# Kernel optimization log

Hardware: AMD Instinct MI355X
Metric: run time of the kernel (lower is better)

The kernel has to match this reference:

```python
import jax, jax.numpy as jnp
import numpy as np

N_IN, N_OUT, D_IN, D_HID, STYLE = 16384, 16384, 64, 256, 64
E = 1048576
EPS_BN = 1e-5
EPS_ADA = 1e-8
SLOPE = 0.2

def leaky(x):
    return jnp.where(x >= 0, x, SLOPE * x)

def bn_train(h, g, b):
    # BatchNorm1d, training mode: batch stats over dim 0, biased variance
    m = jnp.mean(h, axis=0)
    v = jnp.var(h, axis=0)
    return (h - m) * jax.lax.rsqrt(v + EPS_BN) * g + b

def adain(h, style, w1, b1, w2, b2):
    # per-node instance norm over feature axis (unbiased std, as torch.std),
    # style-conditioned per-feature gamma/beta
    mean = jnp.mean(h, axis=1, keepdims=True)
    std = jnp.std(h, axis=1, ddof=1, keepdims=True)
    gamma = w1 @ style + b1
    beta = w2 @ style + b2
    return gamma * (h - mean) / (std + EPS_ADA) + beta

def gat_conv(h, src, dst, W, att_src, att_dst, bias):
    # PyG GATConv, heads=1: linear -> edge attention -> segment softmax -> scatter
    xs = h @ W.T                          # [N, D_IN]
    a_s = xs @ att_src                    # [N]
    a_d = xs @ att_dst                    # [N]
    e = leaky(a_s[src] + a_d[dst])        # [E]
    emax = jax.ops.segment_max(e, dst, num_segments=N_OUT)
    emax = jnp.where(jnp.isfinite(emax), emax, 0.0)
    ex = jnp.exp(e - emax[dst])
    den = jax.ops.segment_sum(ex, dst, num_segments=N_OUT)
    alpha = ex / den[dst]                 # softmax over incoming edges per dst
    out = jax.ops.segment_sum(alpha[:, None] * xs[src], dst, num_segments=N_OUT)
    return out + bias

def setup_inputs():
    key = jax.random.key(0)
    ks = jax.random.split(key, 24)
    p = lambda k, shape: jax.random.normal(k, shape, jnp.float32) * 0.05
    return {
        "x": jax.random.normal(ks[0], (N_IN, D_IN), jnp.float32),
        "style": jax.random.normal(ks[1], (STYLE,), jnp.float32),
        "edge_index": jax.random.randint(ks[2], (2, E), 0, N_OUT, jnp.int32),
        "trs_w": p(ks[3], (N_OUT, N_IN)), "trs_b": jnp.zeros((N_OUT,), jnp.float32),
        "bn2_g": jnp.ones((N_OUT,), jnp.float32), "bn2_b": jnp.zeros((N_OUT,), jnp.float32),
        "fc1_w": p(ks[4], (D_HID, D_IN)), "fc1_b": jnp.zeros((D_HID,), jnp.float32),
        "bn1_g": jnp.ones((D_HID,), jnp.float32), "bn1_b": jnp.zeros((D_HID,), jnp.float32),
        "gat_w": p(ks[5], (D_IN, D_HID)),
        "gat_att_src": p(ks[6], (D_IN,)), "gat_att_dst": p(ks[7], (D_IN,)),
        "gat_b": jnp.zeros((D_IN,), jnp.float32),
        "a1_w1": p(ks[8], (D_IN, STYLE)), "a1_b1": jnp.zeros((D_IN,), jnp.float32),
        "a1_w2": p(ks[9], (D_IN, STYLE)), "a1_b2": jnp.zeros((D_IN,), jnp.float32),
        "a2_w1": p(ks[10], (D_HID, STYLE)), "a2_b1": jnp.zeros((D_HID,), jnp.float32),
        "a2_w2": p(ks[11], (D_HID, STYLE)), "a2_b2": jnp.zeros((D_HID,), jnp.float32),
        "a3_w1": p(ks[12], (D_IN, STYLE)), "a3_b1": jnp.zeros((D_IN,), jnp.float32),
        "a3_w2": p(ks[13], (D_IN, STYLE)), "a3_b2": jnp.zeros((D_IN,), jnp.float32),
    }

def reference(x, style, edge_index, trs_w, trs_b, bn2_g, bn2_b, fc1_w, fc1_b, bn1_g, bn1_b, gat_w, gat_att_src, gat_att_dst, gat_b, a1_w1, a1_b1, a1_w2, a1_b2, a2_w1, a2_b1, a2_w2, a2_b2, a3_w1, a3_b1, a3_w2, a3_b2):
    h = x.T @ trs_w.T + trs_b                 # [D_IN, N_OUT]
    h = leaky(bn_train(h, bn2_g, bn2_b))      # dropout: eval-mode identity
    h = h.T                                    # [N_OUT, D_IN]
    h = adain(h, style, a1_w1, a1_b1, a1_w2, a1_b2)
    h = leaky(bn_train(h @ fc1_w.T + fc1_b, bn1_g, bn1_b))  # [N_OUT, D_HID]
    h = adain(h, style, a2_w1, a2_b1, a2_w2, a2_b2)
    src, dst = edge_index[0], edge_index[1]
    h = leaky(gat_conv(h, src, dst, gat_w, gat_att_src, gat_att_dst, gat_b))
    h = adain(h, style, a3_w1, a3_b1, a3_w2, a3_b2)
    return h
```

## Files before the change

### kernel.cpp

```cpp
#include <hip/hip_runtime.h>
#include <hip/hip_bf16.h>

#define N_NODES 16384
#define NEDGE   1048576

typedef __attribute__((ext_vector_type(4))) float f32x4;
typedef __attribute__((ext_vector_type(4))) unsigned u32x4;
typedef __attribute__((ext_vector_type(8))) short bf16x8;
typedef unsigned short u16;

__device__ __forceinline__ short f2bf(float f) {
  union { float f; unsigned u; } v; v.f = f;
  unsigned r = v.u + 0x7FFFu + ((v.u >> 16) & 1u);
  return (short)(r >> 16);
}
__device__ __forceinline__ unsigned pk2(float lo, float hi) {
  __hip_bfloat162 h = __float22bfloat162_rn(make_float2(lo, hi));
  return *reinterpret_cast<unsigned*>(&h);
}
__device__ __forceinline__ bf16x8 cvt8(f32x4 a, f32x4 b) {
  u32x4 u;
  u[0] = pk2(a[0], a[1]); u[1] = pk2(a[2], a[3]);
  u[2] = pk2(b[0], b[1]); u[3] = pk2(b[2], b[3]);
  return __builtin_bit_cast(bf16x8, u);
}
__device__ __forceinline__ float red16(float v) {
  v += __shfl_xor(v, 1); v += __shfl_xor(v, 2);
  v += __shfl_xor(v, 4); v += __shfl_xor(v, 8);
  return v;
}
__device__ __forceinline__ float red64(float v) {
  v += __shfl_xor(v, 1); v += __shfl_xor(v, 2); v += __shfl_xor(v, 4);
  v += __shfl_xor(v, 8); v += __shfl_xor(v, 16); v += __shfl_xor(v, 32);
  return v;
}
__device__ __forceinline__ float lrelu(float x){ return x >= 0.f ? x : 0.2f*x; }

__global__ __launch_bounds__(256) void k_prep(
    const float* __restrict__ x, const float* __restrict__ style,
    const float* __restrict__ fc1_w, const float* __restrict__ gat_w,
    const float* __restrict__ a1w1, const float* __restrict__ a1b1,
    const float* __restrict__ a1w2, const float* __restrict__ a1b2,
    const float* __restrict__ a2w1, const float* __restrict__ a2b1,
    const float* __restrict__ a2w2, const float* __restrict__ a2b2,
    const float* __restrict__ a3w1, const float* __restrict__ a3b1,
    const float* __restrict__ a3w2, const float* __restrict__ a3b2,
    u16* __restrict__ xpk, u16* __restrict__ fc1pk, u16* __restrict__ gatpk,
    float* __restrict__ gb, int* __restrict__ cnt,
    float* __restrict__ colsum, float* __restrict__ colsq)
{
  int tid = blockIdx.x * 256 + threadIdx.x;
  if (tid < 131072) {
    int lane = tid & 63;
    int kt = tid >> 8, nt = (tid >> 6) & 3;
    int k0 = kt*32 + (lane>>4)*8, c = nt*16 + (lane&15);
    bf16x8 o;
    #pragma unroll
    for (int j = 0; j < 8; ++j) o[j] = f2bf(x[(size_t)(k0+j)*64 + c]);
    ((bf16x8*)xpk)[tid] = o;
  } else if (tid < 133120) {
    int t2 = tid - 131072;
    int lane = t2 & 63, kt = t2 >> 10, nt = (t2 >> 6) & 15;
    int k0 = kt*32 + (lane>>4)*8, c = nt*16 + (lane&15);
    bf16x8 o;
    #pragma unroll
    for (int j = 0; j < 8; ++j) o[j] = f2bf(fc1_w[(size_t)c*64 + k0 + j]);
    ((bf16x8*)fc1pk)[t2] = o;
  } else if (tid < 135168) {
    int t3 = tid - 133120;
    int lane = t3 & 63, kt = t3 >> 8, nt = (t3 >> 6) & 3;
    int k0 = kt*32 + (lane>>4)*8, c = nt*16 + (lane&15);
    bf16x8 o;
    #pragma unroll
    for (int j = 0; j < 8; ++j) o[j] = f2bf(gat_w[(size_t)c*256 + k0 + j]);
    ((bf16x8*)gatpk)[t3] = o;
  } else if (tid < 135936) {
    int t4 = tid - 135168;
    const float* wp; const float* bp; float* op; int d;
    if (t4 < 64)       { wp=a1w1; bp=a1b1; op=gb;       d=t4; }
    else if (t4 < 128) { wp=a1w2; bp=a1b2; op=gb+64;    d=t4-64; }
    else if (t4 < 384) { wp=a2w1; bp=a2b1; op=gb+128;   d=t4-128; }
    else if (t4 < 640) { wp=a2w2; bp=a2b2; op=gb+384;   d=t4-384; }
    else if (t4 < 704) { wp=a3w1; bp=a3b1; op=gb+640;   d=t4-640; }
    else               { wp=a3w2; bp=a3b2; op=gb+704;   d=t4-704; }
    float s = bp[d];
    for (int k = 0; k < 64; ++k) s += wp[(size_t)d*64 + k] * style[k];
    op[d] = s;
  } else if (tid < 152320) {
    cnt[tid - 135936] = 0;
  } else if (tid < 152832) {
    int t6 = tid - 152320;
    if (t6 < 256) colsum[t6] = 0.f; else colsq[t6-256] = 0.f;
  }
}

__global__ __launch_bounds__(256, 4) void k_gemm12(
    const float* __restrict__ W, const u16* __restrict__ xpk,
    const float* __restrict__ trs_b, const float* __restrict__ bn2_g,
    const float* __restrict__ bn2_b, const float* __restrict__ g1,
    const float* __restrict__ be1,
    const u16* __restrict__ fc1pk, const float* __restrict__ fc1_b,
    float* __restrict__ H3, float* __restrict__ colsum, float* __restrict__ colsq,
    const int* __restrict__ dst, int* __restrict__ cnt)
{
  if (blockIdx.x >= 1024) {
    int t = ((blockIdx.x - 1024) << 8) + threadIdx.x;
    #pragma unroll
    for (int i = 0; i < 4; ++i) atomicAdd(&cnt[dst[t + i*262144]], 1);
    return;
  }
  const int lane = threadIdx.x & 63;
  const int wv   = threadIdx.x >> 6;
  const int jb   = blockIdx.x << 4;
  const int c0   = lane & 15, kg = lane >> 4;
  const int kt0  = wv << 7;
  const f32x4* __restrict__ apv =
      (const f32x4*)(W + (size_t)(jb + c0) * 16384 + (size_t)kt0 * 32 + kg * 8);
  const bf16x8* __restrict__ bpv = ((const bf16x8*)xpk) + (size_t)kt0 * 256 + lane;
  f32x4 z = {0.f,0.f,0.f,0.f};
  f32x4 acc0 = z, acc1 = z, acc2 = z, acc3 = z;
  #pragma unroll 2
  for (int t = 0; t < 128; ++t) {
    f32x4 a0 = __builtin_nontemporal_load(apv);
    f32x4 a1 = __builtin_nontemporal_load(apv + 1);
    bf16x8 b0 = bpv[0];
    bf16x8 b1 = bpv[64];
    bf16x8 b2 = bpv[128];
    bf16x8 b3 = bpv[192];
    bf16x8 a = cvt8(a0, a1);
    acc0 = __builtin_amdgcn_mfma_f32_16x16x32_bf16(a, b0, acc0, 0, 0, 0);
    acc1 = __builtin_amdgcn_mfma_f32_16x16x32_bf16(a, b1, acc1, 0, 0, 0);
    acc2 = __builtin_amdgcn_mfma_f32_16x16x32_bf16(a, b2, acc2, 0, 0, 0);
    acc3 = __builtin_amdgcn_mfma_f32_16x16x32_bf16(a, b3, acc3, 0, 0, 0);
    apv += 8; bpv += 256;
  }
  __shared__ float lred[4 * 16 * 64];
  __shared__ float h2t[16 * 68];
  {
    float* rp = lred + (wv << 10) + lane;
    #pragma unroll
    for (int nt = 0; nt < 4; ++nt) {
      f32x4 a = nt==0?acc0:nt==1?acc1:nt==2?acc2:acc3;
      #pragma unroll
      for (int r = 0; r < 4; ++r) rp[((nt<<2)+r)<<6] = a[r];
    }
  }
  __syncthreads();
  if (wv == 0) {
    float val[4][4];
    const float* rp = lred + lane;
    #pragma unroll
    for (int nt = 0; nt < 4; ++nt)
      #pragma unroll
      for (int r = 0; r < 4; ++r) {
        int idx = ((nt<<2)+r)<<6;
        val[nt][r] = rp[idx] + rp[idx+1024] + rp[idx+2048] + rp[idx+3072];
      }
    #pragma unroll
    for (int r = 0; r < 4; ++r) {
      int jr = (kg << 2) + r;
      int j  = jb + jr;
      float tb = trs_b[j];
      float v0 = val[0][r]+tb, v1 = val[1][r]+tb, v2 = val[2][r]+tb, v3 = val[3][r]+tb;
      float s = red16(v0+v1+v2+v3);
      float q = red16(v0*v0+v1*v1+v2*v2+v3*v3);
      float mean = s * 0.015625f;
      float var  = q * 0.015625f - mean*mean;
      float inv  = rsqrtf(var + 1e-5f) * bn2_g[j];
      float bb   = bn2_b[j];
      v0 = lrelu((v0-mean)*inv + bb); v1 = lrelu((v1-mean)*inv + bb);
      v2 = lrelu((v2-mean)*inv + bb); v3 = lrelu((v3-mean)*inv + bb);
      s = red16(v0+v1+v2+v3);
      q = red16(v0*v0+v1*v1+v2*v2+v3*v3);
      mean = s * 0.015625f;
      var  = q * 0.015625f - mean*mean;
      float sd = sqrtf(fmaxf(var, 0.f) * (64.f/63.f));
      float id = 1.f / (sd + 1e-8f);
      float* hr = h2t + jr * 68;
      hr[c0]    = g1[c0]    * (v0-mean)*id + be1[c0];
      hr[c0+16] = g1[c0+16] * (v1-mean)*id + be1[c0+16];
      hr[c0+32] = g1[c0+32] * (v2-mean)*id + be1[c0+32];
      hr[c0+48] = g1[c0+48] * (v3-mean)*id + be1[c0+48];
    }
  }
  __syncthreads();
  const float* ha = h2t + c0 * 68 + (kg << 3);
  bf16x8 a0 = cvt8(*(const f32x4*)ha,        *(const f32x4*)(ha+4));
  bf16x8 a1 = cvt8(*(const f32x4*)(ha+32),   *(const f32x4*)(ha+36));
  const bf16x8* fpv = ((const bf16x8*)fc1pk) + lane;
  f32x4 acc[4] = {z,z,z,z};
  #pragma unroll
  for (int q = 0; q < 4; ++q) {
    int nt = (wv << 2) | q;
    acc[q] = __builtin_amdgcn_mfma_f32_16x16x32_bf16(a0, fpv[nt*64],      acc[q], 0,0,0);
    acc[q] = __builtin_amdgcn_mfma_f32_16x16x32_bf16(a1, fpv[(16+nt)*64], acc[q], 0,0,0);
  }
  #pragma unroll
  for (int q = 0; q < 4; ++q) {
    int c = (((wv << 2) | q) << 4) + c0;
    float bias = fc1_b[c];
    float cs = 0.f, cq = 0.f;
    #pragma unroll
    for (int r = 0; r < 4; ++r) {
      float v = acc[q][r] + bias;
      H3[(size_t)(jb + (kg<<2) + r) * 256 + c] = v;
      cs += v; cq += v*v;
    }
    cs += __shfl_xor(cs, 16); cs += __shfl_xor(cs, 32);
    cq += __shfl_xor(cq, 16); cq += __shfl_xor(cq, 32);
    if (kg == 0) { atomicAdd(&colsum[c], cs); atomicAdd(&colsq[c], cq); }
  }
}

__global__ __launch_bounds__(256) void k_gemm3(
    const float* __restrict__ H3, const float* __restrict__ colsum,
    const float* __restrict__ colsq, const float* __restrict__ bn1_g,
    const float* __restrict__ bn1_b, const float* __restrict__ gb,
    const u16* __restrict__ gatpk,
    const float* __restrict__ att_s, const float* __restrict__ att_d,
    float* __restrict__ xs, float* __restrict__ a_s, float* __restrict__ a_d,
    const int* __restrict__ cnt, int* __restrict__ off, int* __restrict__ cur)
{
  if (blockIdx.x == 1024) {
    __shared__ int ps[256];
    int t = threadIdx.x;
    int base = t * 64;
    int s = 0;
    for (int i = 0; i < 64; ++i) s += cnt[base + i];
    ps[t] = s;
    __syncthreads();
    for (int d = 1; d < 256; d <<= 1) {
      int v = (t >= d) ? ps[t - d] : 0;
      __syncthreads();
      ps[t] += v;
      __syncthreads();
    }
    int run = ps[t] - s;
    for (int i = 0; i < 64; ++i) {
      off[base + i] = run; cur[base + i] = run;
      run += cnt[base + i];
    }
    return;
  }
  const int lane = threadIdx.x & 63, wv = threadIdx.x >> 6;
  const int jb = blockIdx.x << 4;
  const int c0 = lane & 15, kg = lane >> 4;
  const int row = jb + c0;
  const int col0 = (wv << 6) + (kg << 3);
  const float* g2  = gb + 128;
  const float* be2 = gb + 384;

  f32x4 w4[4];
  float ps = 0.f, pq = 0.f;
  #pragma unroll
  for (int kk = 0; kk < 2; ++kk) {
    #pragma unroll
    for (int h = 0; h < 2; ++h) {
      int c = col0 + kk*32 + h*4;
      f32x4 v  = *(const f32x4*)(H3 + (size_t)row*256 + c);
      f32x4 cm = *(const f32x4*)(colsum + c);
      f32x4 cq = *(const f32x4*)(colsq + c);
      f32x4 gg = *(const f32x4*)(bn1_g + c);
      f32x4 bb = *(const f32x4*)(bn1_b + c);
      f32x4 t;
      #pragma unroll
      for (int i = 0; i < 4; ++i) {
        float m  = cm[i] * (1.f/16384.f);
        float va = cq[i] * (1.f/16384.f) - m*m;
        float u  = (v[i]-m) * rsqrtf(va + 1e-5f) * gg[i] + bb[i];
        u = lrelu(u);
        t[i] = u; ps += u; pq += u*u;
      }
      w4[kk*2+h] = t;
    }
  }
  ps += __shfl_xor(ps, 16); ps += __shfl_xor(ps, 32);
  pq += __shfl_xor(pq, 16); pq += __shfl_xor(pq, 32);
  __shared__ float sps[64], sqs[64];
  if (kg == 0) { sps[(wv<<4) + c0] = ps; sqs[(wv<<4) + c0] = pq; }
  __syncthreads();
  float rs = sps[c0] + sps[16+c0] + sps[32+c0] + sps[48+c0];
  float rq = sqs[c0] + sqs[16+c0] + sqs[32+c0] + sqs[48+c0];
  float mean = rs * (1.f/256.f);
  float var  = rq * (1.f/256.f) - mean*mean;
  float sd   = sqrtf(fmaxf(var, 0.f) * (256.f/255.f));
  float id   = 1.f / (sd + 1e-8f);
  bf16x8 afr[2];
  #pragma unroll
  for (int kk = 0; kk < 2; ++kk) {
    f32x4 o[2];
    #pragma unroll
    for (int h = 0; h < 2; ++h) {
      int c = col0 + kk*32 + h*4;
      f32x4 ga = *(const f32x4*)(g2 + c);
      f32x4 bd = *(const f32x4*)(be2 + c);
      #pragma unroll
      for (int i = 0; i < 4; ++i) o[h][i] = ga[i]*(w4[kk*2+h][i]-mean)*id + bd[i];
    }
    afr[kk] = cvt8(o[0], o[1]);
  }
  const bf16x8* bpv = ((const bf16x8*)gatpk) + lane;
  f32x4 z = {0.f,0.f,0.f,0.f};
  f32x4 acc[4] = {z,z,z,z};
  #pragma unroll
  for (int kk = 0; kk < 2; ++kk) {
    int kt = (wv << 1) | kk;
    #pragma unroll
    for (int nt = 0; nt < 4; ++nt)
      acc[nt] = __builtin_amdgcn_mfma_f32_16x16x32_bf16(afr[kk], bpv[((kt<<2)+nt)*64], acc[nt], 0,0,0);
  }
  __shared__ float lred[3 * 16 * 64];
  if (wv) {
    float* rp = lred + ((wv - 1) << 10) + lane;
    #pragma unroll
    for (int nt = 0; nt < 4; ++nt)
      #pragma unroll
      for (int r = 0; r < 4; ++r) rp[((nt<<2)+r)<<6] = acc[nt][r];
  }
  __syncthreads();
  if (wv) return;
  float as0 = att_s[c0], as1 = att_s[c0+16], as2 = att_s[c0+32], as3 = att_s[c0+48];
  float ad0 = att_d[c0], ad1 = att_d[c0+16], ad2 = att_d[c0+32], ad3 = att_d[c0+48];
  const float* rp = lred + lane;
  #pragma unroll
  for (int r = 0; r < 4; ++r) {
    int j = jb + (kg << 2) + r;
    float v[4];
    #pragma unroll
    for (int nt = 0; nt < 4; ++nt) {
      int idx = ((nt<<2)+r)<<6;
      v[nt] = acc[nt][r] + rp[idx] + rp[idx+1024] + rp[idx+2048];
    }
    float* op = xs + (size_t)j * 64 + c0;
    op[0] = v[0]; op[16] = v[1]; op[32] = v[2]; op[48] = v[3];
    float ss = red16(v[0]*as0 + v[1]*as1 + v[2]*as2 + v[3]*as3);
    float dd = red16(v[0]*ad0 + v[1]*ad1 + v[2]*ad2 + v[3]*ad3);
    if (c0 == 0) { a_s[j] = ss; a_d[j] = dd; }
  }
}

__global__ __launch_bounds__(256) void k_scatter(
    const int* __restrict__ src, const int* __restrict__ dst,
    int* __restrict__ cur, int* __restrict__ ssrc)
{
  int t = (blockIdx.x << 8) + threadIdx.x;
  #pragma unroll
  for (int i = 0; i < 4; ++i) {
    int e = t + i * 262144;
    int s = src[e], d = dst[e];
    int p = atomicAdd(&cur[d], 1);
    ssrc[p] = s;
  }
}

__global__ __launch_bounds__(256) void k_gat(
    const int* __restrict__ cnt, const int* __restrict__ off,
    const int* __restrict__ ssrc, const float* __restrict__ a_s,
    const float* __restrict__ a_d,
    const float* __restrict__ xs, const float* __restrict__ gat_b,
    const float* __restrict__ g3, const float* __restrict__ be3,
    float* __restrict__ out)
{
  const int lane = threadIdx.x & 63, wv = threadIdx.x >> 6;
  const int j = (blockIdx.x << 2) | wv;
  const int n = cnt[j], beg = off[j];
  const int c4 = (lane & 15) << 2;
  const int eq = lane >> 4;
  const float adj = a_d[j];
  f32x4 acc = {0.f,0.f,0.f,0.f};
  float den = 0.f;
  if (n > 0) {
    for (int ch = 0; ch < n; ch += 64) {
      int k = ch + lane;
      bool ok = k < n;
      int   s = ok ? ssrc[beg + k] : 0;
      float p = ok ? __expf(lrelu(a_s[s] + adj)) : 0.f;
      den += p;
      int m = n - ch; if (m > 64) m = 64;
      int iters = (m + 3) >> 2;
      for (int i = 0; i < iters; ++i) {
        int idx = (i << 2) | eq;
        float pi = __shfl(p, idx);
        int   si = __shfl(s, idx);
        f32x4 v = *(const f32x4*)(xs + (size_t)si * 64 + c4);
        acc += pi * v;
      }
    }
    den = red64(den);
    #pragma unroll
    for (int i = 0; i < 4; ++i) { acc[i] += __shfl_xor(acc[i], 16); acc[i] += __shfl_xor(acc[i], 32); }
    float rd = 1.f / den;
    acc *= rd;
  }
  f32x4 gbv = *(const f32x4*)(gat_b + c4);
  float v0 = lrelu(acc[0] + gbv[0]);
  float v1 = lrelu(acc[1] + gbv[1]);
  float v2 = lrelu(acc[2] + gbv[2]);
  float v3 = lrelu(acc[3] + gbv[3]);
  float s = red16(v0+v1+v2+v3);
  float q = red16(v0*v0+v1*v1+v2*v2+v3*v3);
  float mean = s * (1.f/64.f);
  float var  = q * (1.f/64.f) - mean*mean;
  float sd   = sqrtf(fmaxf(var, 0.f) * (64.f/63.f));
  float id   = 1.f / (sd + 1e-8f);
  if (eq == 0) {
    f32x4 gv = *(const f32x4*)(g3 + c4);
    f32x4 bv = *(const f32x4*)(be3 + c4);
    f32x4 o;
    o[0] = gv[0]*(v0-mean)*id + bv[0];
    o[1] = gv[1]*(v1-mean)*id + bv[1];
    o[2] = gv[2]*(v2-mean)*id + bv[2];
    o[3] = gv[3]*(v3-mean)*id + bv[3];
    *(f32x4*)(out + (size_t)j * 64 + c4) = o;
  }
}

extern "C" void kernel_launch(void* const* d_in, const int* in_sizes, int n_in,
                              void* d_out, int out_size, void* d_ws, size_t ws_size,
                              hipStream_t stream) {
  (void)in_sizes; (void)n_in; (void)out_size; (void)ws_size;
  const float* x      = (const float*)d_in[0];
  const float* style  = (const float*)d_in[1];
  const int*   ei     = (const int*)d_in[2];
  const float* trs_w  = (const float*)d_in[3];
  const float* trs_b  = (const float*)d_in[4];
  const float* bn2_g  = (const float*)d_in[5];
  const float* bn2_b  = (const float*)d_in[6];
  const float* fc1_w  = (const float*)d_in[7];
  const float* fc1_b  = (const float*)d_in[8];
  const float* bn1_g  = (const float*)d_in[9];
  const float* bn1_b  = (const float*)d_in[10];
  const float* gat_w  = (const float*)d_in[11];
  const float* att_s  = (const float*)d_in[12];
  const float* att_d  = (const float*)d_in[13];
  const float* gat_b  = (const float*)d_in[14];
  const float* a1w1   = (const float*)d_in[15];
  const float* a1b1   = (const float*)d_in[16];
  const float* a1w2   = (const float*)d_in[17];
  const float* a1b2   = (const float*)d_in[18];
  const float* a2w1   = (const float*)d_in[19];
  const float* a2b1   = (const float*)d_in[20];
  const float* a2w2   = (const float*)d_in[21];
  const float* a2b2   = (const float*)d_in[22];
  const float* a3w1   = (const float*)d_in[23];
  const float* a3b1   = (const float*)d_in[24];
  const float* a3w2   = (const float*)d_in[25];
  const float* a3b2   = (const float*)d_in[26];

  char* ws = (char*)d_ws;
  u16*   xpk    = (u16*)(ws);
  u16*   fc1pk  = (u16*)(ws + 2097152);
  u16*   gatpk  = (u16*)(ws + 2129920);
  float* gb     = (float*)(ws + 2162688);
  float* H3     = (float*)(ws + 6361088);
  float* xs     = (float*)(ws + 39915520);
  float* as_    = (float*)(ws + 44109824);
  float* ad_    = (float*)(ws + 44175360);
  float* colsum = (float*)(ws + 44240896);
  float* colsq  = (float*)(ws + 44241920);
  int*   cnt    = (int*)(ws + 44242944);
  int*   off    = (int*)(ws + 44308480);
  int*   cur    = (int*)(ws + 44374016);
  int*   ssrc   = (int*)(ws + 44439552);

  k_prep<<<597, 256, 0, stream>>>(x, style, fc1_w, gat_w,
      a1w1, a1b1, a1w2, a1b2, a2w1, a2b1, a2w2, a2b2, a3w1, a3b1, a3w2, a3b2,
      xpk, fc1pk, gatpk, gb, cnt, colsum, colsq);
  k_gemm12<<<2048, 256, 0, stream>>>(trs_w, xpk, trs_b, bn2_g, bn2_b,
      gb, gb + 64, fc1pk, fc1_b, H3, colsum, colsq, ei + NEDGE, cnt);
  k_gemm3<<<1025, 256, 0, stream>>>(H3, colsum, colsq, bn1_g, bn1_b, gb,
      gatpk, att_s, att_d, xs, as_, ad_, cnt, off, cur);
  k_scatter<<<1024, 256, 0, stream>>>(ei, ei + NEDGE, cur, ssrc);
  k_gat<<<4096, 256, 0, stream>>>(cnt, off, ssrc, as_, ad_, xs, gat_b,
      gb + 640, gb + 704, (float*)d_out);
}
```

Before: 450.9 us.

## Stage trs_w rows through double-buffered swizzled LDS and move degree counting to prep

The first GEMM now has each block load its 16 rows of the 1 GB-class fp32 trs_w matrix with coalesced row-contiguous loads into a double-buffered, XOR-swizzled LDS tile. Each wave then runs one MFMA accumulator over its own 16 output columns, with a block-staggered starting k offset, instead of split-K with four accumulators followed by a cross-wave reduction. The edge in-degree atomics move from the GEMM launch into the prep kernel, and zeroing of the counts and column sums is replaced by hipMemsetAsync calls. The aim is better DRAM access patterns for the bandwidth-bound weight stream, overlap of loads with compute, and less contention from atomics. In exchange it adds a barrier per iteration and two extra memset launches.

```diff
diff --git a/kernel.cpp b/kernel.cpp
--- a/kernel.cpp
+++ b/kernel.cpp
@@ -46,9 +46,14 @@
     const float* __restrict__ a3w1, const float* __restrict__ a3b1,
     const float* __restrict__ a3w2, const float* __restrict__ a3b2,
     u16* __restrict__ xpk, u16* __restrict__ fc1pk, u16* __restrict__ gatpk,
-    float* __restrict__ gb, int* __restrict__ cnt,
-    float* __restrict__ colsum, float* __restrict__ colsq)
+    float* __restrict__ gb, const int* __restrict__ dst, int* __restrict__ cnt)
 {
+  if (blockIdx.x >= 531) {
+    int t = ((blockIdx.x - 531) << 8) + threadIdx.x;
+    #pragma unroll
+    for (int i = 0; i < 4; ++i) atomicAdd(&cnt[dst[t + i*262144]], 1);
+    return;
+  }
   int tid = blockIdx.x * 256 + threadIdx.x;
   if (tid < 131072) {
     int lane = tid & 63;
@@ -86,11 +91,6 @@
     float s = bp[d];
     for (int k = 0; k < 64; ++k) s += wp[(size_t)d*64 + k] * style[k];
     op[d] = s;
-  } else if (tid < 152320) {
-    cnt[tid - 135936] = 0;
-  } else if (tid < 152832) {
-    int t6 = tid - 152320;
-    if (t6 < 256) colsum[t6] = 0.f; else colsq[t6-256] = 0.f;
   }
 }
 
@@ -100,100 +100,109 @@
     const float* __restrict__ bn2_b, const float* __restrict__ g1,
     const float* __restrict__ be1,
     const u16* __restrict__ fc1pk, const float* __restrict__ fc1_b,
-    float* __restrict__ H3, float* __restrict__ colsum, float* __restrict__ colsq,
-    const int* __restrict__ dst, int* __restrict__ cnt)
+    float* __restrict__ H3, float* __restrict__ colsum, float* __restrict__ colsq)
 {
-  if (blockIdx.x >= 1024) {
-    int t = ((blockIdx.x - 1024) << 8) + threadIdx.x;
-    #pragma unroll
-    for (int i = 0; i < 4; ++i) atomicAdd(&cnt[dst[t + i*262144]], 1);
-    return;
-  }
-  const int lane = threadIdx.x & 63;
-  const int wv   = threadIdx.x >> 6;
+  const int tid  = threadIdx.x;
+  const int lane = tid & 63;
+  const int wv   = tid >> 6;
   const int jb   = blockIdx.x << 4;
   const int c0   = lane & 15, kg = lane >> 4;
-  const int kt0  = wv << 7;
-  const f32x4* __restrict__ apv =
-      (const f32x4*)(W + (size_t)(jb + c0) * 16384 + (size_t)kt0 * 32 + kg * 8);
-  const bf16x8* __restrict__ bpv = ((const bf16x8*)xpk) + (size_t)kt0 * 256 + lane;
+  const int sw   = c0 & 7;
+
+  __shared__ __align__(16) float lbuf[2][4096];
+  __shared__ float h2t[16 * 68];
+
+  const float* gsrc[4];
+  int ldst[4];
+  #pragma unroll
+  for (int i = 0; i < 4; ++i) {
+    int r = wv + (i << 2);
+    gsrc[i] = W + (size_t)(jb + r) * 16384 + (size_t)((lane ^ (r & 7)) << 2);
+    ldst[i] = ((r << 6) + lane) << 2;
+  }
+
+  const int it0 = blockIdx.x & 63;
   f32x4 z = {0.f,0.f,0.f,0.f};
-  f32x4 acc0 = z, acc1 = z, acc2 = z, acc3 = z;
-  #pragma unroll 2
-  for (int t = 0; t < 128; ++t) {
-    f32x4 a0 = __builtin_nontemporal_load(apv);
-    f32x4 a1 = __builtin_nontemporal_load(apv + 1);
-    bf16x8 b0 = bpv[0];
-    bf16x8 b1 = bpv[64];
-    bf16x8 b2 = bpv[128];
-    bf16x8 b3 = bpv[192];
-    bf16x8 a = cvt8(a0, a1);
-    acc0 = __builtin_amdgcn_mfma_f32_16x16x32_bf16(a, b0, acc0, 0, 0, 0);
-    acc1 = __builtin_amdgcn_mfma_f32_16x16x32_bf16(a, b1, acc1, 0, 0, 0);
-    acc2 = __builtin_amdgcn_mfma_f32_16x16x32_bf16(a, b2, acc2, 0, 0, 0);
-    acc3 = __builtin_amdgcn_mfma_f32_16x16x32_bf16(a, b3, acc3, 0, 0, 0);
-    apv += 8; bpv += 256;
-  }
-  __shared__ float lred[4 * 16 * 64];
-  __shared__ float h2t[16 * 68];
+  f32x4 acc = z;
+
   {
-    float* rp = lred + (wv << 10) + lane;
-    #pragma unroll
-    for (int nt = 0; nt < 4; ++nt) {
-      f32x4 a = nt==0?acc0:nt==1?acc1:nt==2?acc2:acc3;
-      #pragma unroll
-      for (int r = 0; r < 4; ++r) rp[((nt<<2)+r)<<6] = a[r];
+    int kk = it0 << 8;
+    #pragma unroll
+    for (int i = 0; i < 4; ++i) {
+      f32x4 v = __builtin_nontemporal_load((const f32x4*)(gsrc[i] + kk));
+      *(f32x4*)&lbuf[0][ldst[i]] = v;
     }
   }
   __syncthreads();
-  if (wv == 0) {
-    float val[4][4];
-    const float* rp = lred + lane;
-    #pragma unroll
-    for (int nt = 0; nt < 4; ++nt)
-      #pragma unroll
-      for (int r = 0; r < 4; ++r) {
-        int idx = ((nt<<2)+r)<<6;
-        val[nt][r] = rp[idx] + rp[idx+1024] + rp[idx+2048] + rp[idx+3072];
+
+  const bf16x8* xb = ((const bf16x8*)xpk) + (wv << 6) + lane;
+
+  int buf = 0;
+  for (int it = 0; it < 64; ++it) {
+    f32x4 vn[4];
+    const bool hasNext = (it + 1) < 64;
+    if (hasNext) {
+      int kk = ((it + 1 + it0) & 63) << 8;
+      #pragma unroll
+      for (int i = 0; i < 4; ++i)
+        vn[i] = __builtin_nontemporal_load((const f32x4*)(gsrc[i] + kk));
+    }
+    {
+      int ktg0 = ((it + it0) & 63) << 3;
+      const float* lb = lbuf[buf] + (c0 << 8);
+      const bf16x8* bp = xb + (size_t)ktg0 * 256;
+      #pragma unroll
+      for (int kt = 0; kt < 8; ++kt) {
+        int u0 = (kt << 3) + (kg << 1);
+        f32x4 a0 = *(const f32x4*)(lb + ((u0 ^ sw) << 2));
+        f32x4 a1 = *(const f32x4*)(lb + (((u0 + 1) ^ sw) << 2));
+        bf16x8 b = bp[(size_t)kt << 8];
+        acc = __builtin_amdgcn_mfma_f32_16x16x32_bf16(cvt8(a0, a1), b, acc, 0,0,0);
       }
-    #pragma unroll
-    for (int r = 0; r < 4; ++r) {
-      int jr = (kg << 2) + r;
-      int j  = jb + jr;
-      float tb = trs_b[j];
-      float v0 = val[0][r]+tb, v1 = val[1][r]+tb, v2 = val[2][r]+tb, v3 = val[3][r]+tb;
-      float s = red16(v0+v1+v2+v3);
-      float q = red16(v0*v0+v1*v1+v2*v2+v3*v3);
-      float mean = s * 0.015625f;
-      float var  = q * 0.015625f - mean*mean;
-      float inv  = rsqrtf(var + 1e-5f) * bn2_g[j];
-      float bb   = bn2_b[j];
-      v0 = lrelu((v0-mean)*inv + bb); v1 = lrelu((v1-mean)*inv + bb);
-      v2 = lrelu((v2-mean)*inv + bb); v3 = lrelu((v3-mean)*inv + bb);
-      s = red16(v0+v1+v2+v3);
-      q = red16(v0*v0+v1*v1+v2*v2+v3*v3);
-      mean = s * 0.015625f;
-      var  = q * 0.015625f - mean*mean;
-      float sd = sqrtf(fmaxf(var, 0.f) * (64.f/63.f));
-      float id = 1.f / (sd + 1e-8f);
-      float* hr = h2t + jr * 68;
-      hr[c0]    = g1[c0]    * (v0-mean)*id + be1[c0];
-      hr[c0+16] = g1[c0+16] * (v1-mean)*id + be1[c0+16];
-      hr[c0+32] = g1[c0+32] * (v2-mean)*id + be1[c0+32];
-      hr[c0+48] = g1[c0+48] * (v3-mean)*id + be1[c0+48];
-    }
-  }
+    }
+    if (hasNext) {
+      float* lo = lbuf[buf ^ 1];
+      #pragma unroll
+      for (int i = 0; i < 4; ++i) *(f32x4*)&lo[ldst[i]] = vn[i];
+    }
+    __syncthreads();
+    buf ^= 1;
+  }
+
+  #pragma unroll
+  for (int i = 0; i < 4; ++i)
+    h2t[((kg << 2) + i) * 68 + (wv << 4) + c0] = acc[i];
   __syncthreads();
+
+  #pragma unroll
+  for (int i = 0; i < 4; ++i) {
+    int jr = (wv << 2) + i;
+    int j  = jb + jr;
+    float v = h2t[jr * 68 + lane] + trs_b[j];
+    float s = red64(v), q = red64(v * v);
+    float mean = s * 0.015625f;
+    float var  = q * 0.015625f - mean * mean;
+    float inv  = rsqrtf(var + 1e-5f) * bn2_g[j];
+    v = lrelu((v - mean) * inv + bn2_b[j]);
+    s = red64(v); q = red64(v * v);
+    mean = s * 0.015625f;
+    var  = q * 0.015625f - mean * mean;
+    float sd = sqrtf(fmaxf(var, 0.f) * (64.f / 63.f));
+    float id = 1.f / (sd + 1e-8f);
+    h2t[jr * 68 + lane] = g1[lane] * (v - mean) * id + be1[lane];
+  }
+  __syncthreads();
+
   const float* ha = h2t + c0 * 68 + (kg << 3);
   bf16x8 a0 = cvt8(*(const f32x4*)ha,        *(const f32x4*)(ha+4));
   bf16x8 a1 = cvt8(*(const f32x4*)(ha+32),   *(const f32x4*)(ha+36));
   const bf16x8* fpv = ((const bf16x8*)fc1pk) + lane;
-  f32x4 acc[4] = {z,z,z,z};
+  f32x4 acc2[4] = {z,z,z,z};
   #pragma unroll
   for (int q = 0; q < 4; ++q) {
     int nt = (wv << 2) | q;
-    acc[q] = __builtin_amdgcn_mfma_f32_16x16x32_bf16(a0, fpv[nt*64],      acc[q], 0,0,0);
-    acc[q] = __builtin_amdgcn_mfma_f32_16x16x32_bf16(a1, fpv[(16+nt)*64], acc[q], 0,0,0);
+    acc2[q] = __builtin_amdgcn_mfma_f32_16x16x32_bf16(a0, fpv[nt*64],      acc2[q], 0,0,0);
+    acc2[q] = __builtin_amdgcn_mfma_f32_16x16x32_bf16(a1, fpv[(16+nt)*64], acc2[q], 0,0,0);
   }
   #pragma unroll
   for (int q = 0; q < 4; ++q) {
@@ -202,7 +211,7 @@
     float cs = 0.f, cq = 0.f;
     #pragma unroll
     for (int r = 0; r < 4; ++r) {
-      float v = acc[q][r] + bias;
+      float v = acc2[q][r] + bias;
       H3[(size_t)(jb + (kg<<2) + r) * 256 + c] = v;
       cs += v; cq += v*v;
     }
@@ -463,11 +472,14 @@
   int*   cur    = (int*)(ws + 44374016);
   int*   ssrc   = (int*)(ws + 44439552);
 
-  k_prep<<<597, 256, 0, stream>>>(x, style, fc1_w, gat_w,
+  hipMemsetAsync(colsum, 0, 2048, stream);
+  hipMemsetAsync(cnt, 0, 65536, stream);
+
+  k_prep<<<1555, 256, 0, stream>>>(x, style, fc1_w, gat_w,
       a1w1, a1b1, a1w2, a1b2, a2w1, a2b1, a2w2, a2b2, a3w1, a3b1, a3w2, a3b2,
-      xpk, fc1pk, gatpk, gb, cnt, colsum, colsq);
-  k_gemm12<<<2048, 256, 0, stream>>>(trs_w, xpk, trs_b, bn2_g, bn2_b,
-      gb, gb + 64, fc1pk, fc1_b, H3, colsum, colsq, ei + NEDGE, cnt);
+      xpk, fc1pk, gatpk, gb, ei + NEDGE, cnt);
+  k_gemm12<<<1024, 256, 0, stream>>>(trs_w, xpk, trs_b, bn2_g, bn2_b,
+      gb, gb + 64, fc1pk, fc1_b, H3, colsum, colsq);
   k_gemm3<<<1025, 256, 0, stream>>>(H3, colsum, colsq, bn1_g, bn1_b, gb,
       gatpk, att_s, att_d, xs, as_, ad_, cnt, off, cur);
   k_scatter<<<1024, 256, 0, stream>>>(ei, ei + NEDGE, cur, ssrc);
```

New measurement: 397.3 us. -11.9%, faster.
